# Performance work log

Hardware: AMD Instinct MI355X
Metric: run time of the kernel (lower is better)

## Reference

```python
import jax, jax.numpy as jnp
import numpy as np

B = 4096      # batch (tokens)
H = 1024      # nhid
C = 64        # n_cat
N = 786       # tokens per category (equal n_subclasses)


def setup_inputs() -> dict:
    key = jax.random.key(0)
    k1, k2, k3 = jax.random.split(key, 3)
    initrange = 0.1
    inputs = jax.random.normal(k1, (B, H), dtype=jnp.float32)
    W_top = jax.random.uniform(k2, (H, C), minval=-initrange, maxval=initrange, dtype=jnp.float32)
    b_top = jnp.zeros((C,), dtype=jnp.float32)
    W_bottom = jax.random.uniform(k3, (C, H, N), minval=-initrange, maxval=initrange, dtype=jnp.float32)
    b_bottom = jnp.zeros((C, N), dtype=jnp.float32)
    return {"inputs": inputs, "W_top": W_top, "b_top": b_top,
            "W_bottom": W_bottom, "b_bottom": b_bottom}


def reference(inputs, W_top, b_top, W_bottom, b_bottom):
    # Top-level gating softmax over categories: [B, C]
    top_probs = jax.nn.softmax(inputs @ W_top + b_top, axis=1)
    # Per-category bottom logits, batched over all categories at once: [B, C, N]
    bottom_logits = jnp.einsum('bh,chn->bcn', inputs, W_bottom) + b_bottom
    bottom_probs = jax.nn.softmax(bottom_logits, axis=-1)
    # Scale each category's subclass distribution by its gate prob,
    # then flatten categories in order (matches the original concat order).
    word_probs = top_probs[:, :, None] * bottom_probs  # [B, C, N]
    return word_probs.reshape(B, C * N)
```

## Files before the change

### kernel.cpp

```cpp
#include <hip/hip_runtime.h>
#include <stdint.h>

#define B_  4096
#define H_  1024
#define C_  64
#define N_  786
#define NP_ 896
#define J_  (C_ * N_)
#define BM_ 64
#define BK_ 32

typedef __attribute__((ext_vector_type(4))) float f32x4;
typedef __attribute__((ext_vector_type(8))) short bf16x8;

__device__ __forceinline__ unsigned short f2bf(float f) {
    union { float f; unsigned u; } v; v.f = f;
    unsigned r = v.u + 0x7fffu + ((v.u >> 16) & 1u);
    return (unsigned short)(r >> 16);
}

__device__ __forceinline__ void gload_lds16(const void* g, void* l) {
    __builtin_amdgcn_global_load_lds(
        (const __attribute__((address_space(1))) uint32_t*)g,
        (__attribute__((address_space(3))) uint32_t*)l,
        16, 0, 0);
}

__global__ void k_cast_in(const float* __restrict__ in, unsigned short* __restrict__ out) {
    int i = blockIdx.x * blockDim.x + threadIdx.x;
    float4 v = ((const float4*)in)[i];
    ushort4 o;
    o.x = f2bf(v.x); o.y = f2bf(v.y); o.z = f2bf(v.z); o.w = f2bf(v.w);
    ((ushort4*)out)[i] = o;
}

__global__ void k_wt(const float* __restrict__ w, unsigned short* __restrict__ wt) {
    __shared__ float t[32][33];
    const int c  = blockIdx.z;
    const int h0 = blockIdx.y * 32;
    const int n0 = blockIdx.x * 32;
    const int tx = threadIdx.x, ty = threadIdx.y;
    #pragma unroll
    for (int i = 0; i < 4; ++i) {
        int h = h0 + ty + i * 8;
        int n = n0 + tx;
        float v = (n < N_) ? w[(c * H_ + h) * N_ + n] : 0.0f;
        t[ty + i * 8][tx] = v;
    }
    __syncthreads();
    #pragma unroll
    for (int i = 0; i < 4; ++i) {
        int n = n0 + ty + i * 8;
        int h = h0 + tx;
        wt[((size_t)c * NP_ + n) * H_ + h] = f2bf(t[tx][ty + i * 8]);
    }
}

__global__ void k_top(const float* __restrict__ in, const float* __restrict__ wt,
                      const float* __restrict__ bt, float* __restrict__ top) {
    const int b    = blockIdx.x * 4 + (threadIdx.x >> 6);
    const int lane = threadIdx.x & 63;
    const float* row = in + (size_t)b * H_;
    float acc = bt[lane];
    #pragma unroll 8
    for (int h = 0; h < H_; ++h)
        acc = fmaf(row[h], wt[h * C_ + lane], acc);
    float m = acc;
    for (int d = 32; d; d >>= 1) m = fmaxf(m, __shfl_xor(m, d));
    float e = __expf(acc - m);
    float s = e;
    for (int d = 32; d; d >>= 1) s += __shfl_xor(s, d);
    top[b * C_ + lane] = e / s;
}

__global__ __launch_bounds__(512, 2) void k_main(
    const unsigned short* __restrict__ A,
    const unsigned short* __restrict__ W,
    const float* __restrict__ top,
    const float* __restrict__ bb,
    float* __restrict__ out)
{
    __shared__ unsigned short sA[BM_ * BK_];
    __shared__ unsigned short sB[NP_ * BK_];
    __shared__ float sSum[8 * BM_];
    __shared__ float sScale[BM_];

    const int tid  = threadIdx.x;
    const int w    = tid >> 6;
    const int lane = tid & 63;
    const int b0   = blockIdx.x * BM_;
    const int c    = blockIdx.y;

    f32x4 acc[7][4];
    #pragma unroll
    for (int j = 0; j < 7; ++j)
        #pragma unroll
        for (int mt = 0; mt < 4; ++mt)
            acc[j][mt] = (f32x4)0.0f;

    const int aM = (w < 4) ? (w * 16 + (lane >> 2)) : 0;
    const unsigned short* gA = A + (size_t)(b0 + aM) * H_ + (lane & 3) * 8;
    unsigned short* lA = sA + w * 512;
    const unsigned short* gB0 = W + ((size_t)c * NP_ + w * 112 + (lane >> 2)) * H_ + (lane & 3) * 8;
    unsigned short* lB0 = sB + w * 7 * 512;

    const int ar = lane & 15;
    const int aq = lane >> 4;

    for (int kt = 0; kt < 32; ++kt) {
        __syncthreads();
        if (w < 4) gload_lds16(gA, lA);
        #pragma unroll
        for (int j = 0; j < 7; ++j)
            gload_lds16(gB0 + j * 16 * H_, lB0 + j * 512);
        __syncthreads();

        bf16x8 aF[4];
        #pragma unroll
        for (int mt = 0; mt < 4; ++mt)
            aF[mt] = *(const bf16x8*)(sA + (mt * 16 + ar) * BK_ + aq * 8);
        #pragma unroll
        for (int j = 0; j < 7; ++j) {
            int n = w * 112 + j * 16 + ar;
            bf16x8 bF = *(const bf16x8*)(sB + n * BK_ + aq * 8);
            #pragma unroll
            for (int mt = 0; mt < 4; ++mt)
                acc[j][mt] = __builtin_amdgcn_mfma_f32_16x16x32_bf16(aF[mt], bF, acc[j][mt], 0, 0, 0);
        }
        gA += BK_;
        gB0 += BK_;
    }

    float psum[4][4];
    #pragma unroll
    for (int mt = 0; mt < 4; ++mt)
        #pragma unroll
        for (int r = 0; r < 4; ++r) psum[mt][r] = 0.0f;

    #pragma unroll
    for (int j = 0; j < 7; ++j) {
        int n = w * 112 + j * 16 + ar;
        bool ok = (n < N_);
        float bias = ok ? bb[c * N_ + n] : 0.0f;
        #pragma unroll
        for (int mt = 0; mt < 4; ++mt)
            #pragma unroll
            for (int r = 0; r < 4; ++r) {
                float e = ok ? __expf(acc[j][mt][r] + bias) : 0.0f;
                acc[j][mt][r] = e;
                psum[mt][r] += e;
            }
    }
    #pragma unroll
    for (int d = 1; d < 16; d <<= 1)
        #pragma unroll
        for (int mt = 0; mt < 4; ++mt)
            #pragma unroll
            for (int r = 0; r < 4; ++r)
                psum[mt][r] += __shfl_xor(psum[mt][r], d);
    if (ar == 0) {
        #pragma unroll
        for (int mt = 0; mt < 4; ++mt)
            #pragma unroll
            for (int r = 0; r < 4; ++r)
                sSum[w * 64 + mt * 16 + aq * 4 + r] = psum[mt][r];
    }
    __syncthreads();
    if (tid < 64) {
        float s = 0.0f;
        #pragma unroll
        for (int ww = 0; ww < 8; ++ww) s += sSum[ww * 64 + tid];
        sScale[tid] = top[(b0 + tid) * C_ + c] / s;
    }
    __syncthreads();

    #pragma unroll
    for (int j = 0; j < 7; ++j) {
        int n = w * 112 + j * 16 + ar;
        if (n < N_) {
            #pragma unroll
            for (int mt = 0; mt < 4; ++mt)
                #pragma unroll
                for (int r = 0; r < 4; ++r) {
                    int m = mt * 16 + aq * 4 + r;
                    out[(size_t)(b0 + m) * J_ + c * N_ + n] = acc[j][mt][r] * sScale[m];
                }
        }
    }
}

extern "C" void kernel_launch(void* const* d_in, const int* in_sizes, int n_in,
                              void* d_out, int out_size, void* d_ws, size_t ws_size,
                              hipStream_t stream) {
    const float* in  = (const float*)d_in[0];
    const float* Wt  = (const float*)d_in[1];
    const float* bt  = (const float*)d_in[2];
    const float* Wb  = (const float*)d_in[3];
    const float* bb  = (const float*)d_in[4];
    float* out = (float*)d_out;

    unsigned short* inB = (unsigned short*)d_ws;
    unsigned short* WB  = inB + (size_t)B_ * H_;
    float* top          = (float*)(WB + (size_t)C_ * NP_ * H_);

    k_cast_in<<<(B_ * H_ / 4) / 256, 256, 0, stream>>>(in, inB);
    k_wt<<<dim3(NP_ / 32, H_ / 32, C_), dim3(32, 8), 0, stream>>>(Wb, WB);
    k_top<<<B_ / 4, 256, 0, stream>>>(in, Wt, bt, top);
    k_main<<<dim3(B_ / BM_, C_), 512, 0, stream>>>(inB, WB, top, bb, out);
}
```

Measured before the change: 2.187 ms.

## Double-buffer per-wave B tiles in LDS with swizzle, load A fragments directly

Restructures the k_main K-loop so each wave owns its own double-buffered LDS slice of W rows. The next tile is prefetched with global_load_lds while MFMAs consume the current one, and an explicit vmcnt wait replaces the two block-wide barriers per step. A fragments are loaded straight from global memory into registers, also double-buffered, so the shared A tile is gone. An XOR swizzle of source rows and quads is meant to avoid LDS bank conflicts. The hand-placed waitcnt counts must match the number of issued loads exactly, and the wave-private buffers give up cross-wave reuse of A through LDS.

Result: faster. 1.999 ms (-8.6%).

```diff
diff --git a/kernel.cpp b/kernel.cpp
--- a/kernel.cpp
+++ b/kernel.cpp
@@ -9,6 +9,7 @@
 #define J_  (C_ * N_)
 #define BM_ 64
 #define BK_ 32
+#define WR_ 112
 
 typedef __attribute__((ext_vector_type(4))) float f32x4;
 typedef __attribute__((ext_vector_type(8))) short bf16x8;
@@ -80,16 +81,17 @@
     const float* __restrict__ bb,
     float* __restrict__ out)
 {
-    __shared__ unsigned short sA[BM_ * BK_];
-    __shared__ unsigned short sB[NP_ * BK_];
+    __shared__ unsigned short sB[2][8][WR_ * BK_];
     __shared__ float sSum[8 * BM_];
     __shared__ float sScale[BM_];
 
     const int tid  = threadIdx.x;
     const int w    = tid >> 6;
-    const int lane = tid & 63;
+    const int l    = tid & 63;
     const int b0   = blockIdx.x * BM_;
     const int c    = blockIdx.y;
+    const int ar   = l & 15;
+    const int aq   = l >> 4;
 
     f32x4 acc[7][4];
     #pragma unroll
@@ -98,38 +100,62 @@
         for (int mt = 0; mt < 4; ++mt)
             acc[j][mt] = (f32x4)0.0f;
 
-    const int aM = (w < 4) ? (w * 16 + (lane >> 2)) : 0;
-    const unsigned short* gA = A + (size_t)(b0 + aM) * H_ + (lane & 3) * 8;
-    unsigned short* lA = sA + w * 512;
-    const unsigned short* gB0 = W + ((size_t)c * NP_ + w * 112 + (lane >> 2)) * H_ + (lane & 3) * 8;
-    unsigned short* lB0 = sB + w * 7 * 512;
-
-    const int ar = lane & 15;
-    const int aq = lane >> 4;
-
-    for (int kt = 0; kt < 32; ++kt) {
-        __syncthreads();
-        if (w < 4) gload_lds16(gA, lA);
-        #pragma unroll
-        for (int j = 0; j < 7; ++j)
-            gload_lds16(gB0 + j * 16 * H_, lB0 + j * 512);
-        __syncthreads();
-
-        bf16x8 aF[4];
-        #pragma unroll
-        for (int mt = 0; mt < 4; ++mt)
-            aF[mt] = *(const bf16x8*)(sA + (mt * 16 + ar) * BK_ + aq * 8);
-        #pragma unroll
-        for (int j = 0; j < 7; ++j) {
-            int n = w * 112 + j * 16 + ar;
-            bf16x8 bF = *(const bf16x8*)(sB + n * BK_ + aq * 8);
-            #pragma unroll
-            for (int mt = 0; mt < 4; ++mt)
-                acc[j][mt] = __builtin_amdgcn_mfma_f32_16x16x32_bf16(aF[mt], bF, acc[j][mt], 0, 0, 0);
-        }
-        gA += BK_;
-        gB0 += BK_;
-    }
+    const int srcRow = ((l >> 2) & 14) | (((l >> 2) ^ (l >> 5)) & 1);
+    const int srcQ   = (l & 3) ^ ((l >> 3) & 3);
+    const unsigned short* gB = W + ((size_t)c * NP_ + w * WR_ + srcRow) * H_ + srcQ * 8;
+
+    const unsigned short* gA = A + (size_t)(b0 + ar) * H_ + aq * 8;
+
+    unsigned short* lB0 = &sB[0][w][0];
+    unsigned short* lB1 = &sB[1][w][0];
+
+    bf16x8 aC[4], aN[4];
+
+    #pragma unroll
+    for (int j = 0; j < 7; ++j) gload_lds16(gB + j * (16 * H_), lB0 + j * 512);
+    #pragma unroll
+    for (int mt = 0; mt < 4; ++mt) aC[mt] = *(const bf16x8*)(gA + mt * (16 * H_));
+
+    const unsigned short* gBp = gB + BK_;
+    const unsigned short* gAp = gA + BK_;
+
+#define KSTEP(LRD, LST, ACUR, ANXT)                                              \
+    {                                                                            \
+        _Pragma("unroll")                                                        \
+        for (int j = 0; j < 7; ++j) gload_lds16(gBp + j * (16 * H_), (LST) + j * 512); \
+        _Pragma("unroll")                                                        \
+        for (int mt = 0; mt < 4; ++mt) ANXT[mt] = *(const bf16x8*)(gAp + mt * (16 * H_)); \
+        gBp += BK_; gAp += BK_;                                                  \
+        asm volatile("s_waitcnt vmcnt(11)" ::: "memory");                        \
+        _Pragma("unroll")                                                        \
+        for (int j = 0; j < 7; ++j) {                                            \
+            const int nl = j * 16 + ar;                                          \
+            const int phys = ((nl << 6) | (aq << 4)) ^ (((nl >> 1) & 7) << 4);   \
+            bf16x8 bF = *(const bf16x8*)((const char*)(LRD) + phys);             \
+            _Pragma("unroll")                                                    \
+            for (int mt = 0; mt < 4; ++mt)                                       \
+                acc[j][mt] = __builtin_amdgcn_mfma_f32_16x16x32_bf16(ACUR[mt], bF, acc[j][mt], 0, 0, 0); \
+        }                                                                        \
+    }
+
+    #pragma unroll 1
+    for (int t = 0; t < 15; ++t) {
+        KSTEP(lB0, lB1, aC, aN)
+        KSTEP(lB1, lB0, aN, aC)
+    }
+    KSTEP(lB0, lB1, aC, aN)
+
+    asm volatile("s_waitcnt vmcnt(0)" ::: "memory");
+    #pragma unroll
+    for (int j = 0; j < 7; ++j) {
+        const int nl = j * 16 + ar;
+        const int phys = ((nl << 6) | (aq << 4)) ^ (((nl >> 1) & 7) << 4);
+        bf16x8 bF = *(const bf16x8*)((const char*)lB1 + phys);
+        #pragma unroll
+        for (int mt = 0; mt < 4; ++mt)
+            acc[j][mt] = __builtin_amdgcn_mfma_f32_16x16x32_bf16(aN[mt], bF, acc[j][mt], 0, 0, 0);
+    }
+#undef KSTEP
 
     float psum[4][4];
     #pragma unroll
@@ -139,7 +165,7 @@
 
     #pragma unroll
     for (int j = 0; j < 7; ++j) {
-        int n = w * 112 + j * 16 + ar;
+        int n = w * WR_ + j * 16 + ar;
         bool ok = (n < N_);
         float bias = ok ? bb[c * N_ + n] : 0.0f;
         #pragma unroll
@@ -176,7 +202,7 @@
 
     #pragma unroll
     for (int j = 0; j < 7; ++j) {
-        int n = w * 112 + j * 16 + ar;
+        int n = w * WR_ + j * 16 + ar;
         if (n < N_) {
             #pragma unroll
             for (int mt = 0; mt < 4; ++mt)
```
